# Kernel optimization log

Measured on AMD Instinct MI355X. Metric: run time of the kernel, lower is better.

The kernel has to match this reference:

```python
import jax, jax.numpy as jnp
import numpy as np

TEMPERATURE = 0.5
EPS = 1e-12  # matches torch F.normalize eps


def _l2_normalize(x):
    norm = jnp.linalg.norm(x, axis=-1, keepdims=True)
    return x / jnp.maximum(norm, EPS)


def setup_inputs() -> dict:
    key = jax.random.key(0)
    k1, k2, k3 = jax.random.split(key, 3)
    N, D = 16384, 128
    self_predictions = jax.random.normal(k1, (N, D), dtype=jnp.float32)
    pos_predictions = jax.random.normal(k2, (N, D), dtype=jnp.float32)
    labels1 = jax.random.randint(k3, (N,), 0, 100, dtype=jnp.int64)
    return {
        "self_predictions": self_predictions,
        "pos_predictions": pos_predictions,
        "labels1": labels1,
    }


def reference(self_predictions, pos_predictions, labels1):
    N = labels1.shape[0]
    a = _l2_normalize(self_predictions)  # [N, D]
    b = _l2_normalize(pos_predictions)   # [N, D]
    # cosine similarity of already-normalized rows == dot product (GEMM form)
    sim = jnp.einsum("nd,md->nm", a, b)  # [N, N]
    neg_mask = (labels1[:, None] != labels1[None, :]).astype(sim.dtype)  # 1 - mask
    neg = jnp.exp(-sim / TEMPERATURE) * neg_mask
    return neg.sum() / (N * (N - 1))
```

## Files before the change

### kernel.cpp

```cpp
#include <hip/hip_runtime.h>

typedef unsigned char u8;
typedef unsigned short u16;
typedef float f32x4 __attribute__((ext_vector_type(4)));

#define NROWS 16384
#define DIM 128

#define NEG2LOG2E -2.8853900817779268f

__global__ __launch_bounds__(256) void norm_kernel(
    const float* __restrict__ a, const float* __restrict__ b,
    u8* __restrict__ aO, u8* __restrict__ bO)
{
    int tid  = threadIdx.x;
    int lane = tid & 63;
    int w    = tid >> 6;
    long row = (long)blockIdx.x * 4 + w;

    const float2 va = ((const float2*)(a + row * DIM))[lane];
    float sa = va.x * va.x + va.y * va.y;
    #pragma unroll
    for (int off = 32; off; off >>= 1) sa += __shfl_xor(sa, off, 64);
    float inva = 1.0f / fmaxf(sqrtf(sa), 1e-12f);
    unsigned int pa = (unsigned int)__builtin_amdgcn_cvt_pk_fp8_f32(
        va.x * inva, va.y * inva, 0, false);
    ((u16*)(aO + row * DIM))[lane] = (u16)(pa & 0xffffu);

    const float2 vb = ((const float2*)(b + row * DIM))[lane];
    float sb = vb.x * vb.x + vb.y * vb.y;
    #pragma unroll
    for (int off = 32; off; off >>= 1) sb += __shfl_xor(sb, off, 64);
    float invb = NEG2LOG2E / fmaxf(sqrtf(sb), 1e-12f);
    unsigned int pb = (unsigned int)__builtin_amdgcn_cvt_pk_fp8_f32(
        vb.x * invb, vb.y * invb, 0, false);
    ((u16*)(bO + row * DIM))[lane] = (u16)(pb & 0xffffu);
}

__global__ __launch_bounds__(256, 3) void gemm_kernel(
    const u8* __restrict__ A, const u8* __restrict__ B,
    const int* __restrict__ labels, float* __restrict__ partials)
{
    __shared__ u8 sAB[32768];

    int tid  = threadIdx.x;
    int lane = tid & 63;
    int w    = tid >> 6;
    int wr   = w >> 1;
    int wc   = w & 1;
    int mrow = lane & 15;
    int q    = lane >> 4;

    int rowBase = blockIdx.y * 128;
    int colBase = blockIdx.x * 128;

    {
        int m0 = tid >> 3;
        int p0 = tid & 7;
        int srcOff = m0 * 128 + ((p0 ^ (m0 & 7)) << 4);
        const u8* gpA = A + (size_t)rowBase * DIM + srcOff;
        const u8* gpB = B + (size_t)colBase * DIM + srcOff;
        u8* lp = &sAB[(size_t)tid * 16 - (size_t)lane * 16];
        #pragma unroll
        for (int iter = 0; iter < 4; iter++) {
            __builtin_amdgcn_global_load_lds(
                (const __attribute__((address_space(1))) void*)gpA,
                (__attribute__((address_space(3))) void*)lp, 16, 0, 0);
            __builtin_amdgcn_global_load_lds(
                (const __attribute__((address_space(1))) void*)gpB,
                (__attribute__((address_space(3))) void*)(lp + 16384), 16, 0, 0);
            gpA += 4096; gpB += 4096; lp += 4096;
        }
    }

    int iBase = rowBase + wr * 64 + q * 4;
    int jBase = colBase + wc * 64 + mrow;
    int li[16], lj[4];
    #pragma unroll
    for (int mi = 0; mi < 4; mi++)
        #pragma unroll
        for (int r = 0; r < 4; r++)
            li[mi * 4 + r] = labels[iBase + mi * 16 + r];
    #pragma unroll
    for (int ni = 0; ni < 4; ni++)
        lj[ni] = labels[jBase + ni * 16];

    int aOff[4], bOff[4];
    int qh = (q >> 1), ql = (q & 1) << 3;
    #pragma unroll
    for (int mi = 0; mi < 4; mi++) {
        int m = wr * 64 + mi * 16 + mrow;
        aOff[mi] = m * 128 + ((qh ^ (m & 7)) << 4) + ql;
        int n = wc * 64 + mi * 16 + mrow;
        bOff[mi] = 16384 + n * 128 + ((qh ^ (n & 7)) << 4) + ql;
    }

    f32x4 acc[4][4];
    #pragma unroll
    for (int mi = 0; mi < 4; mi++)
        #pragma unroll
        for (int ni = 0; ni < 4; ni++)
            acc[mi][ni] = (f32x4){0.f, 0.f, 0.f, 0.f};

    __syncthreads();

    #pragma unroll
    for (int ks = 0; ks < 4; ks++) {
        long aF[4], bF[4];
        int x = ks << 5;
        #pragma unroll
        for (int mi = 0; mi < 4; mi++) {
            aF[mi] = *(const long*)(sAB + (aOff[mi] ^ x));
            bF[mi] = *(const long*)(sAB + (bOff[mi] ^ x));
        }
        #pragma unroll
        for (int mi = 0; mi < 4; mi++)
            #pragma unroll
            for (int ni = 0; ni < 4; ni++)
                acc[mi][ni] = __builtin_amdgcn_mfma_f32_16x16x32_fp8_fp8(
                    aF[mi], bF[ni], acc[mi][ni], 0, 0, 0);
    }

    float s0 = 0.0f, s1 = 0.0f;
    #pragma unroll
    for (int mi = 0; mi < 4; mi++)
        #pragma unroll
        for (int ni = 0; ni < 4; ni++)
            #pragma unroll
            for (int r = 0; r < 4; r++) {
                float e = __builtin_amdgcn_exp2f(acc[mi][ni][r]);
                float m = (li[mi * 4 + r] != lj[ni]) ? e : 0.0f;
                if (r & 1) s1 += m; else s0 += m;
            }
    float s = s0 + s1;

    #pragma unroll
    for (int off = 32; off; off >>= 1) s += __shfl_xor(s, off, 64);

    __syncthreads();
    float* red = (float*)sAB;
    if (lane == 0) red[w] = s;
    __syncthreads();
    if (tid == 0) {
        constexpr float SCALE = (float)(1.0 / (16384.0 * 16383.0));
        float t = (red[0] + red[1]) + (red[2] + red[3]);
        partials[blockIdx.y * 128 + blockIdx.x] = t * SCALE;
    }
}

__global__ __launch_bounds__(256) void reduce_kernel(
    const float* __restrict__ partials, float* __restrict__ out)
{
    int tid = threadIdx.x;
    const float4* p4 = (const float4*)partials;
    float s = 0.0f;
    #pragma unroll 4
    for (int i = tid; i < 4096; i += 256) {
        float4 v = p4[i];
        s += (v.x + v.y) + (v.z + v.w);
    }
    #pragma unroll
    for (int off = 32; off; off >>= 1) s += __shfl_xor(s, off, 64);
    __shared__ float red[4];
    if ((tid & 63) == 0) red[tid >> 6] = s;
    __syncthreads();
    if (tid == 0) out[0] = (red[0] + red[1]) + (red[2] + red[3]);
}

extern "C" void kernel_launch(void* const* d_in, const int* in_sizes, int n_in,
                              void* d_out, int out_size, void* d_ws, size_t ws_size,
                              hipStream_t stream) {
    const float* self_p = (const float*)d_in[0];
    const float* pos_p  = (const float*)d_in[1];
    const int*   labels = (const int*)d_in[2];
    float* out = (float*)d_out;

    u8* aB = (u8*)d_ws;
    u8* bB = aB + (size_t)NROWS * DIM;
    float* partials = (float*)(bB + (size_t)NROWS * DIM);

    norm_kernel<<<NROWS / 4, 256, 0, stream>>>(self_p, pos_p, aB, bB);
    gemm_kernel<<<dim3(128, 128), 256, 0, stream>>>(aB, bB, labels, partials);
    reduce_kernel<<<1, 256, 0, stream>>>(partials, out);
}
```

Before: 135.4 us.

## Fuse final reduction via atomics, widen LDS fragment loads, defer label loads

Drops the separate reduce kernel and partials buffer. Each GEMM block now atomically adds its scaled sum into the output, which is zeroed with a memset beforehand. LDS fragment reads are widened to 16-byte vector loads that feed two MFMAs each, halving the number of LDS load instructions. Label loads are moved after the MFMA loop to cut register pressure, and launch bounds are raised to 4 blocks per SM. The trade-off is a non-deterministic float summation order from 16K atomics contending on a single address.

```diff
diff --git a/kernel.cpp b/kernel.cpp
--- a/kernel.cpp
+++ b/kernel.cpp
@@ -3,6 +3,7 @@
 typedef unsigned char u8;
 typedef unsigned short u16;
 typedef float f32x4 __attribute__((ext_vector_type(4)));
+typedef long l2 __attribute__((ext_vector_type(2)));
 
 #define NROWS 16384
 #define DIM 128
@@ -37,9 +38,9 @@
     ((u16*)(bO + row * DIM))[lane] = (u16)(pb & 0xffffu);
 }
 
-__global__ __launch_bounds__(256, 3) void gemm_kernel(
+__global__ __launch_bounds__(256, 4) void gemm_kernel(
     const u8* __restrict__ A, const u8* __restrict__ B,
-    const int* __restrict__ labels, float* __restrict__ partials)
+    const int* __restrict__ labels, float* __restrict__ out)
 {
     __shared__ u8 sAB[32768];
 
@@ -73,26 +74,13 @@
         }
     }
 
-    int iBase = rowBase + wr * 64 + q * 4;
-    int jBase = colBase + wc * 64 + mrow;
-    int li[16], lj[4];
-    #pragma unroll
-    for (int mi = 0; mi < 4; mi++)
-        #pragma unroll
-        for (int r = 0; r < 4; r++)
-            li[mi * 4 + r] = labels[iBase + mi * 16 + r];
-    #pragma unroll
-    for (int ni = 0; ni < 4; ni++)
-        lj[ni] = labels[jBase + ni * 16];
-
     int aOff[4], bOff[4];
-    int qh = (q >> 1), ql = (q & 1) << 3;
     #pragma unroll
     for (int mi = 0; mi < 4; mi++) {
         int m = wr * 64 + mi * 16 + mrow;
-        aOff[mi] = m * 128 + ((qh ^ (m & 7)) << 4) + ql;
+        aOff[mi] = m * 128 + (((q << 1) ^ (m & 7)) << 4);
         int n = wc * 64 + mi * 16 + mrow;
-        bOff[mi] = 16384 + n * 128 + ((qh ^ (n & 7)) << 4) + ql;
+        bOff[mi] = 16384 + n * 128 + (((q << 1) ^ (n & 7)) << 4);
     }
 
     f32x4 acc[4][4];
@@ -105,21 +93,36 @@
     __syncthreads();
 
     #pragma unroll
-    for (int ks = 0; ks < 4; ks++) {
-        long aF[4], bF[4];
-        int x = ks << 5;
+    for (int h = 0; h < 2; h++) {
+        l2 aF[4], bF[4];
+        int x = h << 4;
         #pragma unroll
         for (int mi = 0; mi < 4; mi++) {
-            aF[mi] = *(const long*)(sAB + (aOff[mi] ^ x));
-            bF[mi] = *(const long*)(sAB + (bOff[mi] ^ x));
+            aF[mi] = *(const l2*)(sAB + (aOff[mi] ^ x));
+            bF[mi] = *(const l2*)(sAB + (bOff[mi] ^ x));
         }
         #pragma unroll
         for (int mi = 0; mi < 4; mi++)
             #pragma unroll
-            for (int ni = 0; ni < 4; ni++)
+            for (int ni = 0; ni < 4; ni++) {
                 acc[mi][ni] = __builtin_amdgcn_mfma_f32_16x16x32_fp8_fp8(
-                    aF[mi], bF[ni], acc[mi][ni], 0, 0, 0);
+                    aF[mi][0], bF[ni][0], acc[mi][ni], 0, 0, 0);
+                acc[mi][ni] = __builtin_amdgcn_mfma_f32_16x16x32_fp8_fp8(
+                    aF[mi][1], bF[ni][1], acc[mi][ni], 0, 0, 0);
+            }
     }
+
+    int iBase = rowBase + wr * 64 + q * 4;
+    int jBase = colBase + wc * 64 + mrow;
+    int li[16], lj[4];
+    #pragma unroll
+    for (int mi = 0; mi < 4; mi++)
+        #pragma unroll
+        for (int r = 0; r < 4; r++)
+            li[mi * 4 + r] = labels[iBase + mi * 16 + r];
+    #pragma unroll
+    for (int ni = 0; ni < 4; ni++)
+        lj[ni] = labels[jBase + ni * 16];
 
     float s0 = 0.0f, s1 = 0.0f;
     #pragma unroll
@@ -144,27 +147,8 @@
     if (tid == 0) {
         constexpr float SCALE = (float)(1.0 / (16384.0 * 16383.0));
         float t = (red[0] + red[1]) + (red[2] + red[3]);
-        partials[blockIdx.y * 128 + blockIdx.x] = t * SCALE;
+        atomicAdd(out, t * SCALE);
     }
-}
-
-__global__ __launch_bounds__(256) void reduce_kernel(
-    const float* __restrict__ partials, float* __restrict__ out)
-{
-    int tid = threadIdx.x;
-    const float4* p4 = (const float4*)partials;
-    float s = 0.0f;
-    #pragma unroll 4
-    for (int i = tid; i < 4096; i += 256) {
-        float4 v = p4[i];
-        s += (v.x + v.y) + (v.z + v.w);
-    }
-    #pragma unroll
-    for (int off = 32; off; off >>= 1) s += __shfl_xor(s, off, 64);
-    __shared__ float red[4];
-    if ((tid & 63) == 0) red[tid >> 6] = s;
-    __syncthreads();
-    if (tid == 0) out[0] = (red[0] + red[1]) + (red[2] + red[3]);
 }
 
 extern "C" void kernel_launch(void* const* d_in, const int* in_sizes, int n_in,
@@ -177,9 +161,8 @@
 
     u8* aB = (u8*)d_ws;
     u8* bB = aB + (size_t)NROWS * DIM;
-    float* partials = (float*)(bB + (size_t)NROWS * DIM);
 
+    hipMemsetAsync(out, 0, sizeof(float), stream);
     norm_kernel<<<NROWS / 4, 256, 0, stream>>>(self_p, pos_p, aB, bB);
-    gemm_kernel<<<dim3(128, 128), 256, 0, stream>>>(aB, bB, labels, partials);
-    reduce_kernel<<<1, 256, 0, stream>>>(partials, out);
+    gemm_kernel<<<dim3(128, 128), 256, 0, stream>>>(aB, bB, labels, out);
 }
```

Result: slower. 281.9 us (+108.1%).

## Reuse A tile across four B tiles with double-buffered B loads per block

Applied to the files above, without the earlier changes.

Each block now keeps its 128-row A tile in registers and walks four consecutive 128-column B tiles, prefetching the next B tile into a second LDS buffer while the current one is computed. Fragment loads are widened to 16-byte reads feeding two MFMAs. The grid shrinks by 4x, which cuts A reloads and per-block launch and reduction overhead, and the final reduce reads fewer partials. In exchange each block uses more LDS (48KB), which may lower occupancy, and there are fewer blocks to fill the GPU.

```diff
diff --git a/kernel.cpp b/kernel.cpp
--- a/kernel.cpp
+++ b/kernel.cpp
@@ -3,6 +3,7 @@
 typedef unsigned char u8;
 typedef unsigned short u16;
 typedef float f32x4 __attribute__((ext_vector_type(4)));
+typedef long l2 __attribute__((ext_vector_type(2)));
 
 #define NROWS 16384
 #define DIM 128
@@ -41,7 +42,8 @@
     const u8* __restrict__ A, const u8* __restrict__ B,
     const int* __restrict__ labels, float* __restrict__ partials)
 {
-    __shared__ u8 sAB[32768];
+    __shared__ u8 sA[16384];
+    __shared__ u8 sB[2][16384];
 
     int tid  = threadIdx.x;
     int lane = tid & 63;
@@ -52,99 +54,132 @@
     int q    = lane >> 4;
 
     int rowBase = blockIdx.y * 128;
-    int colBase = blockIdx.x * 128;
+    int colBase = blockIdx.x * 512;
+
+    int m0 = tid >> 3;
+    int p0 = tid & 7;
+    int srcOff = m0 * 128 + ((p0 ^ (m0 & 7)) << 4);
+    int ldsOff = (tid - lane) * 16;
+
+    const u8* gA = A + (size_t)rowBase * DIM + srcOff;
+    const u8* gB = B + (size_t)colBase * DIM + srcOff;
 
     {
-        int m0 = tid >> 3;
-        int p0 = tid & 7;
-        int srcOff = m0 * 128 + ((p0 ^ (m0 & 7)) << 4);
-        const u8* gpA = A + (size_t)rowBase * DIM + srcOff;
-        const u8* gpB = B + (size_t)colBase * DIM + srcOff;
-        u8* lp = &sAB[(size_t)tid * 16 - (size_t)lane * 16];
-        #pragma unroll
-        for (int iter = 0; iter < 4; iter++) {
+        const u8* gpA = gA;
+        const u8* gpB = gB;
+        u8* lpA = &sA[ldsOff];
+        u8* lpB = &sB[0][ldsOff];
+        #pragma unroll
+        for (int it = 0; it < 4; it++) {
             __builtin_amdgcn_global_load_lds(
                 (const __attribute__((address_space(1))) void*)gpA,
-                (__attribute__((address_space(3))) void*)lp, 16, 0, 0);
+                (__attribute__((address_space(3))) void*)lpA, 16, 0, 0);
             __builtin_amdgcn_global_load_lds(
                 (const __attribute__((address_space(1))) void*)gpB,
-                (__attribute__((address_space(3))) void*)(lp + 16384), 16, 0, 0);
-            gpA += 4096; gpB += 4096; lp += 4096;
+                (__attribute__((address_space(3))) void*)lpB, 16, 0, 0);
+            gpA += 4096; gpB += 4096; lpA += 4096; lpB += 4096;
         }
     }
 
     int iBase = rowBase + wr * 64 + q * 4;
-    int jBase = colBase + wc * 64 + mrow;
-    int li[16], lj[4];
+    int li[16];
     #pragma unroll
     for (int mi = 0; mi < 4; mi++)
         #pragma unroll
         for (int r = 0; r < 4; r++)
             li[mi * 4 + r] = labels[iBase + mi * 16 + r];
-    #pragma unroll
-    for (int ni = 0; ni < 4; ni++)
-        lj[ni] = labels[jBase + ni * 16];
 
     int aOff[4], bOff[4];
-    int qh = (q >> 1), ql = (q & 1) << 3;
     #pragma unroll
     for (int mi = 0; mi < 4; mi++) {
         int m = wr * 64 + mi * 16 + mrow;
-        aOff[mi] = m * 128 + ((qh ^ (m & 7)) << 4) + ql;
+        aOff[mi] = m * 128 + (((q << 1) ^ (m & 7)) << 4);
         int n = wc * 64 + mi * 16 + mrow;
-        bOff[mi] = 16384 + n * 128 + ((qh ^ (n & 7)) << 4) + ql;
-    }
-
-    f32x4 acc[4][4];
-    #pragma unroll
-    for (int mi = 0; mi < 4; mi++)
+        bOff[mi] = n * 128 + (((q << 1) ^ (n & 7)) << 4);
+    }
+
+    __syncthreads();
+
+    l2 aF[2][4];
+    #pragma unroll
+    for (int h = 0; h < 2; h++)
+        #pragma unroll
+        for (int mi = 0; mi < 4; mi++)
+            aF[h][mi] = *(const l2*)(sA + (aOff[mi] ^ (h << 4)));
+
+    float s = 0.0f;
+
+    #pragma unroll
+    for (int jt = 0; jt < 4; jt++) {
+        if (jt < 3) {
+            const u8* gp = gB + (jt + 1) * (128 * DIM);
+            u8* lp = &sB[(jt + 1) & 1][ldsOff];
+            #pragma unroll
+            for (int it = 0; it < 4; it++) {
+                __builtin_amdgcn_global_load_lds(
+                    (const __attribute__((address_space(1))) void*)gp,
+                    (__attribute__((address_space(3))) void*)lp, 16, 0, 0);
+                gp += 4096; lp += 4096;
+            }
+        }
+
+        int jBase = colBase + jt * 128 + wc * 64 + mrow;
+        int lj[4];
         #pragma unroll
         for (int ni = 0; ni < 4; ni++)
-            acc[mi][ni] = (f32x4){0.f, 0.f, 0.f, 0.f};
-
-    __syncthreads();
-
-    #pragma unroll
-    for (int ks = 0; ks < 4; ks++) {
-        long aF[4], bF[4];
-        int x = ks << 5;
-        #pragma unroll
-        for (int mi = 0; mi < 4; mi++) {
-            aF[mi] = *(const long*)(sAB + (aOff[mi] ^ x));
-            bF[mi] = *(const long*)(sAB + (bOff[mi] ^ x));
+            lj[ni] = labels[jBase + ni * 16];
+
+        const u8* sb = sB[jt & 1];
+        f32x4 acc[4][4];
+        #pragma unroll
+        for (int mi = 0; mi < 4; mi++)
+            #pragma unroll
+            for (int ni = 0; ni < 4; ni++)
+                acc[mi][ni] = (f32x4){0.f, 0.f, 0.f, 0.f};
+
+        #pragma unroll
+        for (int h = 0; h < 2; h++) {
+            l2 bF[4];
+            #pragma unroll
+            for (int ni = 0; ni < 4; ni++)
+                bF[ni] = *(const l2*)(sb + (bOff[ni] ^ (h << 4)));
+            #pragma unroll
+            for (int mi = 0; mi < 4; mi++)
+                #pragma unroll
+                for (int ni = 0; ni < 4; ni++) {
+                    acc[mi][ni] = __builtin_amdgcn_mfma_f32_16x16x32_fp8_fp8(
+                        aF[h][mi][0], bF[ni][0], acc[mi][ni], 0, 0, 0);
+                    acc[mi][ni] = __builtin_amdgcn_mfma_f32_16x16x32_fp8_fp8(
+                        aF[h][mi][1], bF[ni][1], acc[mi][ni], 0, 0, 0);
+                }
         }
+
+        float s0 = 0.0f, s1 = 0.0f;
         #pragma unroll
         for (int mi = 0; mi < 4; mi++)
             #pragma unroll
             for (int ni = 0; ni < 4; ni++)
-                acc[mi][ni] = __builtin_amdgcn_mfma_f32_16x16x32_fp8_fp8(
-                    aF[mi], bF[ni], acc[mi][ni], 0, 0, 0);
-    }
-
-    float s0 = 0.0f, s1 = 0.0f;
-    #pragma unroll
-    for (int mi = 0; mi < 4; mi++)
-        #pragma unroll
-        for (int ni = 0; ni < 4; ni++)
-            #pragma unroll
-            for (int r = 0; r < 4; r++) {
-                float e = __builtin_amdgcn_exp2f(acc[mi][ni][r]);
-                float m = (li[mi * 4 + r] != lj[ni]) ? e : 0.0f;
-                if (r & 1) s1 += m; else s0 += m;
-            }
-    float s = s0 + s1;
+                #pragma unroll
+                for (int r = 0; r < 4; r++) {
+                    float e = __builtin_amdgcn_exp2f(acc[mi][ni][r]);
+                    float m = (li[mi * 4 + r] != lj[ni]) ? e : 0.0f;
+                    if (r & 1) s1 += m; else s0 += m;
+                }
+        s += s0 + s1;
+
+        __syncthreads();
+    }
 
     #pragma unroll
     for (int off = 32; off; off >>= 1) s += __shfl_xor(s, off, 64);
 
-    __syncthreads();
-    float* red = (float*)sAB;
+    float* red = (float*)sA;
     if (lane == 0) red[w] = s;
     __syncthreads();
     if (tid == 0) {
         constexpr float SCALE = (float)(1.0 / (16384.0 * 16383.0));
         float t = (red[0] + red[1]) + (red[2] + red[3]);
-        partials[blockIdx.y * 128 + blockIdx.x] = t * SCALE;
+        partials[blockIdx.y * 32 + blockIdx.x] = t * SCALE;
     }
 }
 
@@ -155,7 +190,7 @@
     const float4* p4 = (const float4*)partials;
     float s = 0.0f;
     #pragma unroll 4
-    for (int i = tid; i < 4096; i += 256) {
+    for (int i = tid; i < 1024; i += 256) {
         float4 v = p4[i];
         s += (v.x + v.y) + (v.z + v.w);
     }
@@ -180,6 +215,6 @@
     float* partials = (float*)(bB + (size_t)NROWS * DIM);
 
     norm_kernel<<<NROWS / 4, 256, 0, stream>>>(self_p, pos_p, aB, bB);
-    gemm_kernel<<<dim3(128, 128), 256, 0, stream>>>(aB, bB, labels, partials);
+    gemm_kernel<<<dim3(32, 128), 256, 0, stream>>>(aB, bB, labels, partials);
     reduce_kernel<<<1, 256, 0, stream>>>(partials, out);
 }
```

Result: faster. 129.2 us (-4.6%).
